# Kernel tuning notes

Measured on AMD Instinct MI355X. Metric: run time of the kernel, lower is better.

The kernel has to match this reference:

```python
import jax, jax.numpy as jnp
import numpy as np


def _conv(x, w, b, pad):
    y = jax.lax.conv_general_dilated(x, w, window_strides=(1, 1),
                                     padding=[(pad, pad), (pad, pad)],
                                     dimension_numbers=('NCHW', 'OIHW', 'NCHW'))
    return y + b[None, :, None, None]


def _kernel_normalizer(mask, k):
    # softmax over the k*k kernel taps; hamming=1 so the renorm is a numerical no-op (kept faithful)
    n, mck2, h, w = mask.shape
    mc = mck2 // (k * k)
    m = jax.nn.softmax(mask.reshape(n, mc, k * k, h, w), axis=2)
    m = m / jnp.sum(m, axis=2, keepdims=True)
    return m.reshape(n, mck2, h, w)


def _carafe(feat, mask, k, g, s):
    # CARAFE: out[n,c,i,j] = sum_{ki,kj} mask[n, grp*k*k + ki*k + kj, i, j] * feat[n, c, i//s+ki-r, j//s+kj-r]
    n, c, h, w = feat.shape
    r = (k - 1) // 2
    cg = c // g
    hs, ws = h * s, w * s
    pad = jnp.pad(feat, ((0, 0), (0, 0), (r, r), (r, r)))
    m = mask.reshape(n, g, k * k, hs, ws)
    out = jnp.zeros((n, g, cg, hs, ws), feat.dtype)
    idx = 0
    for ki in range(k):
        for kj in range(k):
            sh = pad[:, :, ki:ki + h, kj:kj + w]
            if s > 1:
                sh = jnp.repeat(jnp.repeat(sh, s, axis=2), s, axis=3)
            out = out + sh.reshape(n, g, cg, hs, ws) * m[:, :, idx][:, :, None]
            idx += 1
    return out.reshape(n, c, hs, ws)


def setup_inputs() -> dict:
    key = jax.random.key(0)
    ks = jax.random.split(key, 8)
    N, CH, CL, H, W, CC = 4, 256, 256, 128, 128, 64
    KL, KH, EK = 5, 3, 3

    def w_init(k, shape):
        fan_in = shape[1] * shape[2] * shape[3]
        return jax.random.normal(k, shape, jnp.float32) * (1.0 / np.sqrt(fan_in))

    return {
        'hr_feat': jax.random.normal(ks[0], (N, CH, H, W), jnp.float32),
        'lr_feat': jax.random.normal(ks[1], (N, CL, H // 2, W // 2), jnp.float32),
        'hr_w': w_init(ks[2], (CC, CH, 1, 1)), 'hr_b': jnp.zeros((CC,), jnp.float32),
        'lr_w': w_init(ks[3], (CC, CL, 1, 1)), 'lr_b': jnp.zeros((CC,), jnp.float32),
        'enc_w': w_init(ks[4], (KL * KL, CC, EK, EK)), 'enc_b': jnp.zeros((KL * KL,), jnp.float32),
        'enc2_w': w_init(ks[5], (KH * KH, CC, EK, EK)), 'enc2_b': jnp.zeros((KH * KH,), jnp.float32),
    }


def reference(hr_feat, lr_feat, hr_w, hr_b, lr_w, lr_b, enc_w, enc_b, enc2_w, enc2_b):
    KL, KH, G = 5, 3, 1
    chf = _conv(hr_feat, hr_w, hr_b, 0)
    clf = _conv(lr_feat, lr_w, lr_b, 0)
    mask_hr_hr = _conv(chf, enc2_w, enc2_b, 1)
    mask_hr_init = _kernel_normalizer(mask_hr_hr, KH)
    chf = chf + chf - _carafe(chf, mask_hr_init, KH, G, 1)
    mask_lr_hr = _conv(chf, enc_w, enc_b, 1)
    mask_lr_init = _kernel_normalizer(mask_lr_hr, KL)
    mask_lr_lr_lr = _conv(clf, enc_w, enc_b, 1)
    # carafe scale-2 output is already hr-sized -> F.interpolate(nearest, hr size) is identity
    mask_lr_lr = _carafe(mask_lr_lr_lr, mask_lr_init, KL, G, 2)
    mask_lr = mask_lr_hr + mask_lr_lr
    mask_lr_init = _kernel_normalizer(mask_lr, KL)
    mask_hr_lr = _carafe(_conv(clf, enc2_w, enc2_b, 1), mask_lr_init, KL, G, 2)
    mask_hr = mask_hr_hr + mask_hr_lr
    mask_lr_out = _kernel_normalizer(mask_lr, KL)
    lr_out = _carafe(lr_feat, mask_lr_out, KL, G, 2)
    mask_hr_out = _kernel_normalizer(mask_hr, KH)
    hr_out = (hr_feat - _carafe(hr_feat, mask_hr_out, KH, G, 1)) + hr_feat
    return (mask_lr_out, hr_out, lr_out)
```

## Files before the change

### kernel.cpp

```cpp
#include <hip/hip_runtime.h>
#include <hip/hip_bf16.h>

typedef __hip_bfloat16 bf16;

constexpr int Nn  = 4;
constexpr int Ci  = 256;
constexpr int Cc  = 64;
constexpr int Hh  = 128;
constexpr int Ww  = 128;
constexpr int HWh = Hh * Ww;
constexpr int Hl  = 64;
constexpr int Wl  = 64;
constexpr int HWl = Hl * Wl;
constexpr int K2L = 25;
constexpr int K2H = 9;

constexpr size_t OFF_MASK = 0;
constexpr size_t OFF_HR   = (size_t)Nn * K2L * HWh;
constexpr size_t OFF_LR   = OFF_HR + (size_t)Nn * Ci * HWh;

constexpr size_t A_CHF    = 0;
constexpr size_t A_MLRHR  = 0;
constexpr size_t A_MLRLL  = 4300000;
constexpr size_t A_CLFE2  = 4800000;
constexpr size_t A_MHRRAW = 5000000;
constexpr size_t A_WHR    = 7800000;
constexpr size_t A_WLR    = 7820000;
constexpr size_t A_WENC   = 7840000;
constexpr size_t A_WENC2  = 7860000;
constexpr size_t A_BHR    = 7870000;
constexpr size_t A_BLR    = 7870100;
constexpr size_t A_BENC   = 7870200;
constexpr size_t A_BENC2  = 7870300;

constexpr size_t B_CLF    = 0;
constexpr size_t B_CHF2   = 1100000;
constexpr size_t B_MHRHR  = 5300000;
constexpr size_t B_MLR    = 0;

__device__ __forceinline__ float tofloat(float v) { return v; }
__device__ __forceinline__ float tofloat(bf16 v) { return __bfloat162float(v); }

template<typename T> __device__ __forceinline__ T fromfloat(float v);
template<> __device__ __forceinline__ float fromfloat<float>(float v) { return v; }
template<> __device__ __forceinline__ bf16  fromfloat<bf16>(float v)  { return __float2bfloat16(v); }

__device__ __forceinline__ float* scrp(void* d, int f32, size_t reg, size_t off) {
  float* b = f32 ? ((float*)d + reg) : (float*)((bf16*)d + reg);
  return b + off;
}

__global__ void detect_dtype(const void* feat, int* flag) {
  __shared__ int s;
  if (threadIdx.x == 0) s = 0;
  __syncthreads();
  unsigned short b = ((const unsigned short*)feat)[threadIdx.x];
  float v = __uint_as_float(((unsigned int)b) << 16);
  if (!(fabsf(v) < 1000.0f)) atomicOr(&s, 1);
  __syncthreads();
  if (threadIdx.x == 0) *flag = s;
}

template<typename T>
__device__ void prep_body(const T* hw, const T* hb, const T* lw, const T* lb,
                          const T* ew, const T* eb, const T* e2w, const T* e2b,
                          float* whr, float* wlr, float* wenc, float* wenc2,
                          float* bhr, float* blr, float* benc, float* benc2) {
  int tid = blockIdx.x * 256 + threadIdx.x, nt = gridDim.x * 256;
  for (int i = tid; i < Cc * Ci; i += nt) {
    int co = i / Ci, ci = i % Ci;
    whr[ci * Cc + co] = tofloat(hw[i]);
    wlr[ci * Cc + co] = tofloat(lw[i]);
  }
  for (int i = tid; i < K2L * Cc * 9; i += nt) {
    int ko = i / (Cc * 9), r = i % (Cc * 9), ci = r / 9, k = r % 9;
    wenc[(ci * K2L + ko) * 9 + k] = tofloat(ew[i]);
  }
  for (int i = tid; i < K2H * Cc * 9; i += nt) {
    int ko = i / (Cc * 9), r = i % (Cc * 9), ci = r / 9, k = r % 9;
    wenc2[(ci * K2H + ko) * 9 + k] = tofloat(e2w[i]);
  }
  if (tid < Cc)  { bhr[tid] = tofloat(hb[tid]); blr[tid] = tofloat(lb[tid]); }
  if (tid < K2L) benc[tid]  = tofloat(eb[tid]);
  if (tid < K2H) benc2[tid] = tofloat(e2b[tid]);
}

__global__ void prep_weights(const int* flag, void* dout,
                             const void* hw, const void* hb, const void* lw, const void* lb,
                             const void* ew, const void* eb, const void* e2w, const void* e2b) {
  int f32 = *flag;
  float* whr   = scrp(dout, f32, OFF_LR, A_WHR);
  float* wlr   = scrp(dout, f32, OFF_LR, A_WLR);
  float* wenc  = scrp(dout, f32, OFF_LR, A_WENC);
  float* wenc2 = scrp(dout, f32, OFF_LR, A_WENC2);
  float* bhr   = scrp(dout, f32, OFF_LR, A_BHR);
  float* blr   = scrp(dout, f32, OFF_LR, A_BLR);
  float* benc  = scrp(dout, f32, OFF_LR, A_BENC);
  float* benc2 = scrp(dout, f32, OFF_LR, A_BENC2);
  if (f32) prep_body<float>((const float*)hw, (const float*)hb, (const float*)lw, (const float*)lb,
                            (const float*)ew, (const float*)eb, (const float*)e2w, (const float*)e2b,
                            whr, wlr, wenc, wenc2, bhr, blr, benc, benc2);
  else     prep_body<bf16>((const bf16*)hw, (const bf16*)hb, (const bf16*)lw, (const bf16*)lb,
                           (const bf16*)ew, (const bf16*)eb, (const bf16*)e2w, (const bf16*)e2b,
                           whr, wlr, wenc, wenc2, bhr, blr, benc, benc2);
}

template<typename T, int CW>
__device__ __forceinline__ void conv1x1_core(const T* __restrict__ in, const float* __restrict__ wt,
                                             const float* __restrict__ bias, float* __restrict__ out,
                                             int P, int n, int pbase, int co0) {
  const T* inp = in + (size_t)n * Ci * P + pbase;
  float acc0[CW], acc1[CW];
  #pragma unroll
  for (int c = 0; c < CW; ++c) { float b = bias[co0 + c]; acc0[c] = b; acc1[c] = b; }

  #pragma unroll 8
  for (int ci = 0; ci < Ci; ++ci) {
    float v0, v1;
    if (sizeof(T) == 2) {
      unsigned u = *reinterpret_cast<const unsigned*>(inp + (size_t)ci * P);
      v0 = __uint_as_float(u << 16);
      v1 = __uint_as_float(u & 0xffff0000u);
    } else {
      float2 f = *reinterpret_cast<const float2*>(inp + (size_t)ci * P);
      v0 = f.x; v1 = f.y;
    }
    const float* wr = wt + ci * Cc + co0;
    #pragma unroll
    for (int c = 0; c < CW; ++c) {
      float wv = wr[c];
      acc0[c] = fmaf(v0, wv, acc0[c]);
      acc1[c] = fmaf(v1, wv, acc1[c]);
    }
  }
  float* op = out + (size_t)n * Cc * P + pbase;
  #pragma unroll
  for (int c = 0; c < CW; ++c)
    *reinterpret_cast<float2*>(op + (size_t)(co0 + c) * P) = make_float2(acc0[c], acc1[c]);
}

template<int CW>
__global__ __launch_bounds__(256) void conv1x1_k(const int* flag, void* dout, const void* in,
                                                 size_t w_off, size_t b_off,
                                                 size_t o_reg, size_t o_off, int P) {
  int f32 = __builtin_amdgcn_readfirstlane(*flag);
  const float* wt   = scrp(dout, f32, OFF_LR, w_off);
  const float* bias = scrp(dout, f32, OFF_LR, b_off);
  float* out        = scrp(dout, f32, o_reg, o_off);
  const int tid = threadIdx.x;
  const int n = blockIdx.z;
  const int pbase = (blockIdx.x * 64 + (tid & 63)) * 2;
  const int co0 = __builtin_amdgcn_readfirstlane(blockIdx.y * 4 * CW + (tid >> 6) * CW);
  if (f32) conv1x1_core<float, CW>((const float*)in, wt, bias, out, P, n, pbase, co0);
  else     conv1x1_core<bf16, CW>((const bf16*)in, wt, bias, out, P, n, pbase, co0);
}

constexpr int STG_TOT = 16 * 324;
constexpr int NSTG    = 21;

template<int KO, int KOG>
__device__ __forceinline__ void conv3x3_body(const float* __restrict__ in,
                                             const float* __restrict__ wt,
                                             const float* __restrict__ bias,
                                             float* __restrict__ out,
                                             int hh, int ww, int n, int ko0,
                                             int bx, int by, float* tile) {
  const int tid = threadIdx.x;
  const int tx = tid & 15, ty = tid >> 4;
  const bool inter = (bx >= 16) && (by >= 16) && (bx + 32 <= ww) && (by + 32 <= hh);

  float acc[KOG];
  #pragma unroll
  for (int ko = 0; ko < KOG; ++ko) acc[ko] = bias[ko0 + ko];

  float rg[NSTG];
  #pragma unroll
  for (int j = 0; j < NSTG; ++j) {
    int i = tid + j * 256;
    if (i < STG_TOT) {
      int ci = i / 324, r = i % 324, yy = r / 18, xx = r % 18;
      int gy = by + yy - 1, gx = bx + xx - 1;
      float v = 0.f;
      if (inter || (gy >= 0 && gy < hh && gx >= 0 && gx < ww))
        v = in[(((size_t)n * Cc + ci) * hh + gy) * ww + gx];
      rg[j] = v;
    }
  }

  for (int cc = 0; cc < Cc; cc += 16) {
    __syncthreads();
    #pragma unroll
    for (int j = 0; j < NSTG; ++j) {
      int i = tid + j * 256;
      if (i < STG_TOT) tile[i] = rg[j];
    }
    __syncthreads();
    if (cc + 16 < Cc) {
      #pragma unroll
      for (int j = 0; j < NSTG; ++j) {
        int i = tid + j * 256;
        if (i < STG_TOT) {
          int ci = i / 324, r = i % 324, yy = r / 18, xx = r % 18;
          int gy = by + yy - 1, gx = bx + xx - 1;
          float v = 0.f;
          if (inter || (gy >= 0 && gy < hh && gx >= 0 && gx < ww))
            v = in[(((size_t)n * Cc + cc + 16 + ci) * hh + gy) * ww + gx];
          rg[j] = v;
        }
      }
    }
    for (int ci = 0; ci < 16; ++ci) {
      float nb[9];
      #pragma unroll
      for (int dy = 0; dy < 3; ++dy)
        #pragma unroll
        for (int dx = 0; dx < 3; ++dx)
          nb[dy * 3 + dx] = tile[ci * 324 + (ty + dy) * 18 + tx + dx];
      const float* wr = wt + ((size_t)(cc + ci) * KO + ko0) * 9;
      #pragma unroll
      for (int ko = 0; ko < KOG; ++ko)
        #pragma unroll
        for (int k = 0; k < 9; ++k)
          acc[ko] = fmaf(wr[ko * 9 + k], nb[k], acc[ko]);
    }
  }
  const size_t ob = (((size_t)n * KO + ko0) * hh + by + ty) * ww + bx + tx;
  #pragma unroll
  for (int ko = 0; ko < KOG; ++ko) out[ob + (size_t)ko * hh * ww] = acc[ko];
}

template<int KO, int KOG>
__global__ __launch_bounds__(256) void conv3x3_k(const int* flag, void* dout,
                                                 size_t i_reg, size_t i_off,
                                                 size_t w_off, size_t b_off,
                                                 size_t o_reg, size_t o_off, int hh, int ww) {
  const int f32 = __builtin_amdgcn_readfirstlane(*flag);
  const float* in   = scrp(dout, f32, i_reg, i_off);
  const float* wt   = scrp(dout, f32, OFF_LR, w_off);
  const float* bias = scrp(dout, f32, OFF_LR, b_off);
  float* out        = scrp(dout, f32, o_reg, o_off);

  constexpr int NG = KO / KOG;
  __shared__ float tile[STG_TOT];
  const int n = blockIdx.z / NG;
  const int ko0 = (blockIdx.z % NG) * KOG;
  conv3x3_body<KO, KOG>(in, wt, bias, out, hh, ww, n, ko0, blockIdx.x * 16, blockIdx.y * 16, tile);
}

__global__ __launch_bounds__(256) void conv3x3_dual_k(const int* flag, void* dout) {
  const int f32 = __builtin_amdgcn_readfirstlane(*flag);
  const float* clf   = scrp(dout, f32, OFF_HR, B_CLF);
  const float* wenc  = scrp(dout, f32, OFF_LR, A_WENC);
  const float* benc  = scrp(dout, f32, OFF_LR, A_BENC);
  const float* wenc2 = scrp(dout, f32, OFF_LR, A_WENC2);
  const float* benc2 = scrp(dout, f32, OFF_LR, A_BENC2);
  float* o_ll = scrp(dout, f32, OFF_LR, A_MLRLL);
  float* o_e2 = scrp(dout, f32, OFF_LR, A_CLFE2);
  __shared__ float tile[STG_TOT];
  const int z = blockIdx.z;
  const int g = z & 7, n = z >> 3;
  const int bx = blockIdx.x * 16, by = blockIdx.y * 16;
  if (g < 5) conv3x3_body<K2L, 5>(clf, wenc, benc, o_ll, Hl, Wl, n, g * 5, bx, by, tile);
  else       conv3x3_body<K2H, 3>(clf, wenc2, benc2, o_e2, Hl, Wl, n, (g - 5) * 3, bx, by, tile);
}

template<typename FT, typename OT, int FINAL, int SM>
__device__ void carafe1_body(const FT* __restrict__ feat, const float* __restrict__ mask,
                             void* dout, size_t out_reg, float* outscr, int C, int CPB) {
  const int tid = threadIdx.x;
  const int tx = tid & 15, ty = tid >> 4;
  const int bx = blockIdx.x * 16, by = blockIdx.y * 16;
  const int numCG = C / CPB;
  const int n = blockIdx.z / numCG, cg = blockIdx.z % numCG;
  const int x = bx + tx, y = by + ty;
  const bool inter = (bx >= 16) && (by >= 16) && (bx + 32 <= Ww) && (by + 32 <= Hh);

  float mv[9];
  #pragma unroll
  for (int k = 0; k < 9; ++k)
    mv[k] = mask[(((size_t)n * 9 + k) * Hh + y) * Ww + x];
  if (SM) {
    float m = -1e30f;
    #pragma unroll
    for (int k = 0; k < 9; ++k) m = fmaxf(m, mv[k]);
    float s = 0.f;
    #pragma unroll
    for (int k = 0; k < 9; ++k) { mv[k] = __expf(mv[k] - m); s += mv[k]; }
    const float inv = 1.0f / s;
    #pragma unroll
    for (int k = 0; k < 9; ++k) mv[k] *= inv;
  }

  const int c0 = cg * CPB;
  if (inter) {
    for (int c = c0; c < c0 + CPB; ++c) {
      const FT* fp = feat + ((size_t)n * C + c) * HWh + (size_t)y * Ww + x;
      float center = tofloat(fp[0]);
      float s = 0.f;
      #pragma unroll
      for (int dy = -1; dy <= 1; ++dy)
        #pragma unroll
        for (int dx = -1; dx <= 1; ++dx)
          s = fmaf(tofloat(fp[dy * Ww + dx]), mv[(dy + 1) * 3 + (dx + 1)], s);
      float r = 2.f * center - s;
      const size_t li = ((size_t)n * C + c) * HWh + (size_t)y * Ww + x;
      if (FINAL) ((OT*)dout)[out_reg + li] = fromfloat<OT>(r);
      else       outscr[li] = r;
    }
  } else {
    for (int c = c0; c < c0 + CPB; ++c) {
      const FT* fp = feat + ((size_t)n * C + c) * HWh;
      float s = 0.f, center = 0.f;
      #pragma unroll
      for (int dy = -1; dy <= 1; ++dy)
        #pragma unroll
        for (int dx = -1; dx <= 1; ++dx) {
          int yy = y + dy, xx = x + dx;
          float fv = 0.f;
          if (yy >= 0 && yy < Hh && xx >= 0 && xx < Ww) fv = tofloat(fp[yy * Ww + xx]);
          if (dy == 0 && dx == 0) center = fv;
          s = fmaf(fv, mv[(dy + 1) * 3 + (dx + 1)], s);
        }
      float r = 2.f * center - s;
      const size_t li = ((size_t)n * C + c) * HWh + (size_t)y * Ww + x;
      if (FINAL) ((OT*)dout)[out_reg + li] = fromfloat<OT>(r);
      else       outscr[li] = r;
    }
  }
}

__global__ __launch_bounds__(256) void carafe1_scr_k(const int* flag, void* dout,
    size_t f_reg, size_t f_off, size_t m_reg, size_t m_off, size_t o_reg, size_t o_off,
    int C, int CPB) {
  int f32 = __builtin_amdgcn_readfirstlane(*flag);
  carafe1_body<float, float, 0, 1>(scrp(dout, f32, f_reg, f_off), scrp(dout, f32, m_reg, m_off),
                                   dout, 0, scrp(dout, f32, o_reg, o_off), C, CPB);
}

__global__ __launch_bounds__(256) void carafe1_io_k(const int* flag, void* dout, const void* feat,
    size_t m_reg, size_t m_off, size_t out_reg, int C, int CPB) {
  int f32 = __builtin_amdgcn_readfirstlane(*flag);
  const float* m = scrp(dout, f32, m_reg, m_off);
  if (f32) carafe1_body<float, float, 1, 1>((const float*)feat, m, dout, out_reg, nullptr, C, CPB);
  else     carafe1_body<bf16, bf16, 1, 1>((const bf16*)feat, m, dout, out_reg, nullptr, C, CPB);
}

template<typename FT, typename MT, typename OT, typename MOT, int ADD, int FINAL, int SM, int WMASK>
__device__ void carafe2_body(const FT* __restrict__ feat, const MT* __restrict__ mask,
                             const float* __restrict__ addend, void* dout, size_t out_reg,
                             float* outscr, int C, int CPB) {
  __shared__ float ft[8][144];
  const int tid = threadIdx.x;
  const int tx = tid & 15, ty = tid >> 4;
  const int bx = blockIdx.x * 16, by = blockIdx.y * 16;
  const int numCG = C / CPB;
  const int n = blockIdx.z / numCG, cg = blockIdx.z % numCG;
  const int x = bx + tx, y = by + ty;
  const bool inter = (bx >= 16) && (by >= 16) && (bx + 32 <= Ww) && (by + 32 <= Hh);

  float mv[25];
  #pragma unroll
  for (int k = 0; k < 25; ++k)
    mv[k] = tofloat(mask[(((size_t)n * 25 + k) * Hh + y) * Ww + x]);
  if (SM) {
    float m = -1e30f;
    #pragma unroll
    for (int k = 0; k < 25; ++k) m = fmaxf(m, mv[k]);
    float s = 0.f;
    #pragma unroll
    for (int k = 0; k < 25; ++k) { mv[k] = __expf(mv[k] - m); s += mv[k]; }
    const float inv = 1.0f / s;
    #pragma unroll
    for (int k = 0; k < 25; ++k) mv[k] *= inv;
  }
  if (WMASK && cg == 0) {
    const size_t g = (size_t)n * 25 * HWh + (size_t)y * Ww + x;
    MOT* mo = (MOT*)dout;
    #pragma unroll
    for (int k = 0; k < 25; ++k) mo[g + (size_t)k * HWh] = fromfloat<MOT>(mv[k]);
  }

  const int fy0 = (by >> 1) - 2, fx0 = (bx >> 1) - 2;
  const int fyb = (ty >> 1) + 2, fxb = (tx >> 1) + 2;
  const int c0 = cg * CPB;

  for (int cb = 0; cb < CPB; cb += 8) {
    const int lim = (CPB - cb < 8) ? (CPB - cb) : 8;
    __syncthreads();
    if (inter) {
      for (int i = tid; i < lim * 144; i += 256) {
        int cc = i / 144, r = i % 144, fy = r / 12, fx = r % 12;
        ft[cc][r] = tofloat(feat[((size_t)n * C + c0 + cb + cc) * HWl + (fy0 + fy) * Wl + fx0 + fx]);
      }
    } else {
      for (int i = tid; i < lim * 144; i += 256) {
        int cc = i / 144, r = i % 144, fy = r / 12, fx = r % 12;
        int gy = fy0 + fy, gx = fx0 + fx;
        float v = 0.f;
        if (gy >= 0 && gy < Hl && gx >= 0 && gx < Wl)
          v = tofloat(feat[((size_t)n * C + c0 + cb + cc) * HWl + gy * Wl + gx]);
        ft[cc][r] = v;
      }
    }
    __syncthreads();
    for (int cc = 0; cc < lim; ++cc) {
      float s = 0.f;
      #pragma unroll
      for (int ki = 0; ki < 5; ++ki)
        #pragma unroll
        for (int kj = 0; kj < 5; ++kj)
          s = fmaf(ft[cc][(fyb + ki - 2) * 12 + (fxb + kj - 2)], mv[ki * 5 + kj], s);
      const size_t li = (((size_t)n * C + c0 + cb + cc) * Hh + y) * Ww + x;
      float r = ADD ? (addend[li] + s) : s;
      if (FINAL) ((OT*)dout)[out_reg + li] = fromfloat<OT>(r);
      else       outscr[li] = r;
    }
  }
}

__global__ __launch_bounds__(256) void carafe2_scr_k(const int* flag, void* dout,
    size_t f_reg, size_t f_off, size_t m_reg, size_t m_off, size_t a_reg, size_t a_off,
    size_t o_reg, size_t o_off, int C, int CPB) {
  int f32 = __builtin_amdgcn_readfirstlane(*flag);
  carafe2_body<float, float, float, float, 1, 0, 1, 0>(
      scrp(dout, f32, f_reg, f_off), scrp(dout, f32, m_reg, m_off),
      scrp(dout, f32, a_reg, a_off), dout, 0, scrp(dout, f32, o_reg, o_off), C, CPB);
}

__global__ __launch_bounds__(256) void carafe2_m0_k(const int* flag, void* dout,
    size_t f_reg, size_t f_off, size_t m_reg, size_t m_off, size_t a_reg, size_t a_off,
    size_t o_reg, size_t o_off, int C, int CPB) {
  int f32 = __builtin_amdgcn_readfirstlane(*flag);
  const float* f = scrp(dout, f32, f_reg, f_off);
  const float* m = scrp(dout, f32, m_reg, m_off);
  const float* a = scrp(dout, f32, a_reg, a_off);
  float* o = scrp(dout, f32, o_reg, o_off);
  if (f32) carafe2_body<float, float, float, float, 1, 0, 1, 1>(f, m, a, dout, 0, o, C, CPB);
  else     carafe2_body<float, float, float, bf16, 1, 0, 1, 1>(f, m, a, dout, 0, o, C, CPB);
}

__global__ __launch_bounds__(256) void carafe2_io_k(const int* flag, void* dout, const void* feat,
    size_t out_reg, int C, int CPB) {
  int f32 = __builtin_amdgcn_readfirstlane(*flag);
  if (f32) carafe2_body<float, float, float, float, 0, 1, 0, 0>((const float*)feat, (const float*)dout,
      nullptr, dout, out_reg, nullptr, C, CPB);
  else     carafe2_body<bf16, bf16, bf16, bf16, 0, 1, 0, 0>((const bf16*)feat, (const bf16*)dout,
      nullptr, dout, out_reg, nullptr, C, CPB);
}

extern "C" void kernel_launch(void* const* d_in, const int* in_sizes, int n_in,
                              void* d_out, int out_size, void* d_ws, size_t ws_size,
                              hipStream_t stream) {
  const void* hr_feat = d_in[0];
  const void* lr_feat = d_in[1];
  int* flag = (int*)d_ws;

  detect_dtype<<<1, 256, 0, stream>>>(hr_feat, flag);
  prep_weights<<<64, 256, 0, stream>>>(flag, d_out, d_in[2], d_in[3], d_in[4], d_in[5],
                                       d_in[6], d_in[7], d_in[8], d_in[9]);
  conv1x1_k<8><<<dim3(HWh / 128, 2, Nn), 256, 0, stream>>>(flag, d_out, hr_feat, A_WHR, A_BHR, OFF_LR, A_CHF, HWh);
  conv1x1_k<4><<<dim3(HWl / 128, 4, Nn), 256, 0, stream>>>(flag, d_out, lr_feat, A_WLR, A_BLR, OFF_HR, B_CLF, HWl);
  conv3x3_k<K2H, 3><<<dim3(8, 8, Nn * 3), 256, 0, stream>>>(flag, d_out, OFF_LR, A_CHF, A_WENC2, A_BENC2, OFF_HR, B_MHRHR, Hh, Ww);
  conv3x3_dual_k<<<dim3(4, 4, Nn * 8), 256, 0, stream>>>(flag, d_out);
  carafe1_scr_k<<<dim3(8, 8, Nn * (Cc / 16)), 256, 0, stream>>>(flag, d_out, OFF_LR, A_CHF, OFF_HR, B_MHRHR, OFF_HR, B_CHF2, Cc, 16);
  conv3x3_k<K2L, 5><<<dim3(8, 8, Nn * 5), 256, 0, stream>>>(flag, d_out, OFF_HR, B_CHF2, A_WENC, A_BENC, OFF_LR, A_MLRHR, Hh, Ww);
  carafe2_scr_k<<<dim3(8, 8, Nn * 5), 256, 0, stream>>>(flag, d_out, OFF_LR, A_MLRLL, OFF_LR, A_MLRHR,
                                                        OFF_LR, A_MLRHR, OFF_HR, B_MLR, K2L, 5);
  carafe2_m0_k<<<dim3(8, 8, Nn * 3), 256, 0, stream>>>(flag, d_out, OFF_LR, A_CLFE2,
                                                       OFF_HR, B_MLR, OFF_HR, B_MHRHR,
                                                       OFF_LR, A_MHRRAW, K2H, 3);
  carafe1_io_k<<<dim3(8, 8, Nn * (Ci / 32)), 256, 0, stream>>>(flag, d_out, hr_feat,
                                                               OFF_LR, A_MHRRAW, OFF_HR, Ci, 32);
  carafe2_io_k<<<dim3(8, 8, Nn * (Ci / 32)), 256, 0, stream>>>(flag, d_out, lr_feat, OFF_LR, Ci, 32);
}
```

Before: 537.1 us.

## Rewrite final CARAFE kernels to compute two pixels per thread with vector I/O

Replaces the two final-output CARAFE kernels with new versions in which each thread computes two horizontally adjacent output pixels. Feature, mask and output accesses use packed float2 or paired-bf16 loads and stores. The 3x3 kernel reads rows straight from global memory. The 5x5 scale-2 kernel stages a wider low-res tile in shared memory and shares each feature value between both pixels. The grids are reshaped to 32x16 tiles with 16 channels per block, which raises bytes per memory transaction and halves per-pixel mask and softmax overhead, at the cost of more registers per thread.

New measurement: 546.2 us. Within noise of the previous version (+1.7%).

```diff
diff --git a/kernel.cpp b/kernel.cpp
--- a/kernel.cpp
+++ b/kernel.cpp
@@ -44,6 +44,10 @@
 template<typename T> __device__ __forceinline__ T fromfloat(float v);
 template<> __device__ __forceinline__ float fromfloat<float>(float v) { return v; }
 template<> __device__ __forceinline__ bf16  fromfloat<bf16>(float v)  { return __float2bfloat16(v); }
+
+__device__ __forceinline__ unsigned short bfbits(bf16 v) {
+  return *reinterpret_cast<unsigned short*>(&v);
+}
 
 __device__ __forceinline__ float* scrp(void* d, int f32, size_t reg, size_t off) {
   float* b = f32 ? ((float*)d + reg) : (float*)((bf16*)d + reg);
@@ -337,12 +341,114 @@
                                    dout, 0, scrp(dout, f32, o_reg, o_off), C, CPB);
 }
 
-__global__ __launch_bounds__(256) void carafe1_io_k(const int* flag, void* dout, const void* feat,
+template<typename FT>
+__device__ void carafe1_io2_body(const FT* __restrict__ feat, const float* __restrict__ mask,
+                                 FT* __restrict__ outp, int C, int CPB) {
+  const int tid = threadIdx.x;
+  const int tx = tid & 15, ty = tid >> 4;
+  const int bx = blockIdx.x * 32, by = blockIdx.y * 16;
+  const int numCG = C / CPB;
+  const int n = blockIdx.z / numCG, cg = blockIdx.z % numCG;
+  const int x0 = bx + 2 * tx, y = by + ty;
+  const bool inter = (bx >= 2) && (by >= 1) && (bx + 34 <= Ww) && (by + 17 <= Hh);
+
+  float mv0[9], mv1[9];
+  #pragma unroll
+  for (int k = 0; k < 9; ++k) {
+    float2 m2 = *reinterpret_cast<const float2*>(mask + (((size_t)n * 9 + k) * Hh + y) * Ww + x0);
+    mv0[k] = m2.x; mv1[k] = m2.y;
+  }
+  {
+    float m = -1e30f;
+    #pragma unroll
+    for (int k = 0; k < 9; ++k) m = fmaxf(m, mv0[k]);
+    float s = 0.f;
+    #pragma unroll
+    for (int k = 0; k < 9; ++k) { mv0[k] = __expf(mv0[k] - m); s += mv0[k]; }
+    const float inv = 1.0f / s;
+    #pragma unroll
+    for (int k = 0; k < 9; ++k) mv0[k] *= inv;
+  }
+  {
+    float m = -1e30f;
+    #pragma unroll
+    for (int k = 0; k < 9; ++k) m = fmaxf(m, mv1[k]);
+    float s = 0.f;
+    #pragma unroll
+    for (int k = 0; k < 9; ++k) { mv1[k] = __expf(mv1[k] - m); s += mv1[k]; }
+    const float inv = 1.0f / s;
+    #pragma unroll
+    for (int k = 0; k < 9; ++k) mv1[k] *= inv;
+  }
+
+  const int c0 = cg * CPB;
+  if (inter) {
+    for (int c = c0; c < c0 + CPB; ++c) {
+      const FT* fp = feat + ((size_t)n * C + c) * HWh;
+      float s0 = 0.f, s1 = 0.f, c0v = 0.f, c1v = 0.f;
+      #pragma unroll
+      for (int dy = -1; dy <= 1; ++dy) {
+        const FT* rp = fp + (size_t)(y + dy) * Ww + x0 - 2;
+        float v[6];
+        if (sizeof(FT) == 2) {
+          const unsigned* up = reinterpret_cast<const unsigned*>(rp);
+          unsigned u0 = up[0], u1 = up[1], u2 = up[2];
+          v[0] = __uint_as_float(u0 << 16); v[1] = __uint_as_float(u0 & 0xffff0000u);
+          v[2] = __uint_as_float(u1 << 16); v[3] = __uint_as_float(u1 & 0xffff0000u);
+          v[4] = __uint_as_float(u2 << 16); v[5] = __uint_as_float(u2 & 0xffff0000u);
+        } else {
+          const float2* qp = reinterpret_cast<const float2*>(rp);
+          float2 a = qp[0], b = qp[1], cq = qp[2];
+          v[0] = a.x; v[1] = a.y; v[2] = b.x; v[3] = b.y; v[4] = cq.x; v[5] = cq.y;
+        }
+        if (dy == 0) { c0v = v[2]; c1v = v[3]; }
+        #pragma unroll
+        for (int dx = 0; dx < 3; ++dx) {
+          s0 = fmaf(v[1 + dx], mv0[(dy + 1) * 3 + dx], s0);
+          s1 = fmaf(v[2 + dx], mv1[(dy + 1) * 3 + dx], s1);
+        }
+      }
+      float r0 = 2.f * c0v - s0, r1 = 2.f * c1v - s1;
+      const size_t li = ((size_t)n * C + c) * HWh + (size_t)y * Ww + x0;
+      if (sizeof(FT) == 2) {
+        bf16 b0 = __float2bfloat16(r0), b1 = __float2bfloat16(r1);
+        *reinterpret_cast<unsigned*>(outp + li) =
+            (unsigned)bfbits(b0) | ((unsigned)bfbits(b1) << 16);
+      } else {
+        *reinterpret_cast<float2*>(outp + li) = make_float2(r0, r1);
+      }
+    }
+  } else {
+    for (int c = c0; c < c0 + CPB; ++c) {
+      const FT* fp = feat + ((size_t)n * C + c) * HWh;
+      #pragma unroll
+      for (int px = 0; px < 2; ++px) {
+        const int x = x0 + px;
+        float s = 0.f, center = 0.f;
+        #pragma unroll
+        for (int dy = -1; dy <= 1; ++dy)
+          #pragma unroll
+          for (int dx = -1; dx <= 1; ++dx) {
+            int yy = y + dy, xx = x + dx;
+            float fv = 0.f;
+            if (yy >= 0 && yy < Hh && xx >= 0 && xx < Ww) fv = tofloat(fp[yy * Ww + xx]);
+            if (dy == 0 && dx == 0) center = fv;
+            float mw = px ? mv1[(dy + 1) * 3 + (dx + 1)] : mv0[(dy + 1) * 3 + (dx + 1)];
+            s = fmaf(fv, mw, s);
+          }
+        float r = 2.f * center - s;
+        outp[((size_t)n * C + c) * HWh + (size_t)y * Ww + x] = fromfloat<FT>(r);
+      }
+    }
+  }
+}
+
+__global__ __launch_bounds__(256) void carafe1_io2_k(const int* flag, void* dout, const void* feat,
     size_t m_reg, size_t m_off, size_t out_reg, int C, int CPB) {
   int f32 = __builtin_amdgcn_readfirstlane(*flag);
   const float* m = scrp(dout, f32, m_reg, m_off);
-  if (f32) carafe1_body<float, float, 1, 1>((const float*)feat, m, dout, out_reg, nullptr, C, CPB);
-  else     carafe1_body<bf16, bf16, 1, 1>((const bf16*)feat, m, dout, out_reg, nullptr, C, CPB);
+  if (f32) carafe1_io2_body<float>((const float*)feat, m, (float*)dout + out_reg, C, CPB);
+  else     carafe1_io2_body<bf16>((const bf16*)feat, m, (bf16*)dout + out_reg, C, CPB);
 }
 
 template<typename FT, typename MT, typename OT, typename MOT, int ADD, int FINAL, int SM, int WMASK>
@@ -439,13 +545,93 @@
   else     carafe2_body<float, float, float, bf16, 1, 0, 1, 1>(f, m, a, dout, 0, o, C, CPB);
 }
 
-__global__ __launch_bounds__(256) void carafe2_io_k(const int* flag, void* dout, const void* feat,
+template<typename FT>
+__device__ void carafe2_io2_body(const FT* __restrict__ feat, const FT* __restrict__ maskO,
+                                 FT* __restrict__ outp, int C, int CPB) {
+  __shared__ float ft[8][240];
+  const int tid = threadIdx.x;
+  const int tx = tid & 15, ty = tid >> 4;
+  const int bx = blockIdx.x * 32, by = blockIdx.y * 16;
+  const int numCG = C / CPB;
+  const int n = blockIdx.z / numCG, cg = blockIdx.z % numCG;
+  const int x0 = bx + 2 * tx, y = by + ty;
+
+  float mv0[25], mv1[25];
+  #pragma unroll
+  for (int k = 0; k < 25; ++k) {
+    const FT* mp = maskO + (((size_t)n * 25 + k) * Hh + y) * Ww + x0;
+    if (sizeof(FT) == 2) {
+      unsigned u = *reinterpret_cast<const unsigned*>(mp);
+      mv0[k] = __uint_as_float(u << 16);
+      mv1[k] = __uint_as_float(u & 0xffff0000u);
+    } else {
+      float2 m2 = *reinterpret_cast<const float2*>(mp);
+      mv0[k] = m2.x; mv1[k] = m2.y;
+    }
+  }
+
+  const int fy0 = (by >> 1) - 2, fx0 = (bx >> 1) - 2;
+  const int fyb = (ty >> 1) + 2, fxc = tx + 2;
+  const int c0 = cg * CPB;
+  const bool stg_ok = (fy0 >= 0) && (fy0 + 12 <= Hl) && (fx0 >= 0) && (fx0 + 20 <= Wl);
+
+  for (int cb = 0; cb < CPB; cb += 8) {
+    const int lim = (CPB - cb < 8) ? (CPB - cb) : 8;
+    __syncthreads();
+    if (stg_ok) {
+      for (int i = tid; i < lim * 120; i += 256) {
+        int cc = i / 120, r = i % 120, fy = r / 10, fx2 = (r % 10) * 2;
+        const FT* sp = feat + ((size_t)n * C + c0 + cb + cc) * HWl + (size_t)(fy0 + fy) * Wl + fx0 + fx2;
+        float a, b;
+        if (sizeof(FT) == 2) {
+          unsigned u = *reinterpret_cast<const unsigned*>(sp);
+          a = __uint_as_float(u << 16);
+          b = __uint_as_float(u & 0xffff0000u);
+        } else {
+          float2 f2 = *reinterpret_cast<const float2*>(sp);
+          a = f2.x; b = f2.y;
+        }
+        ft[cc][fy * 20 + fx2]     = a;
+        ft[cc][fy * 20 + fx2 + 1] = b;
+      }
+    } else {
+      for (int i = tid; i < lim * 240; i += 256) {
+        int cc = i / 240, r = i % 240, fy = r / 20, fx = r % 20;
+        int gy = fy0 + fy, gx = fx0 + fx;
+        float v = 0.f;
+        if (gy >= 0 && gy < Hl && gx >= 0 && gx < Wl)
+          v = tofloat(feat[((size_t)n * C + c0 + cb + cc) * HWl + (size_t)gy * Wl + gx]);
+        ft[cc][r] = v;
+      }
+    }
+    __syncthreads();
+    for (int cc = 0; cc < lim; ++cc) {
+      float s0 = 0.f, s1 = 0.f;
+      #pragma unroll
+      for (int ki = 0; ki < 5; ++ki)
+        #pragma unroll
+        for (int kj = 0; kj < 5; ++kj) {
+          float fv = ft[cc][(fyb + ki - 2) * 20 + (fxc + kj - 2)];
+          s0 = fmaf(fv, mv0[ki * 5 + kj], s0);
+          s1 = fmaf(fv, mv1[ki * 5 + kj], s1);
+        }
+      const size_t li = (((size_t)n * C + c0 + cb + cc) * Hh + y) * Ww + x0;
+      if (sizeof(FT) == 2) {
+        bf16 b0 = __float2bfloat16(s0), b1 = __float2bfloat16(s1);
+        *reinterpret_cast<unsigned*>(outp + li) =
+            (unsigned)bfbits(b0) | ((unsigned)bfbits(b1) << 16);
+      } else {
+        *reinterpret_cast<float2*>(outp + li) = make_float2(s0, s1);
+      }
+    }
+  }
+}
+
+__global__ __launch_bounds__(256) void carafe2_io2_k(const int* flag, void* dout, const void* feat,
     size_t out_reg, int C, int CPB) {
   int f32 = __builtin_amdgcn_readfirstlane(*flag);
-  if (f32) carafe2_body<float, float, float, float, 0, 1, 0, 0>((const float*)feat, (const float*)dout,
-      nullptr, dout, out_reg, nullptr, C, CPB);
-  else     carafe2_body<bf16, bf16, bf16, bf16, 0, 1, 0, 0>((const bf16*)feat, (const bf16*)dout,
-      nullptr, dout, out_reg, nullptr, C, CPB);
+  if (f32) carafe2_io2_body<float>((const float*)feat, (const float*)dout, (float*)dout + out_reg, C, CPB);
+  else     carafe2_io2_body<bf16>((const bf16*)feat, (const bf16*)dout, (bf16*)dout + out_reg, C, CPB);
 }
 
 extern "C" void kernel_launch(void* const* d_in, const int* in_sizes, int n_in,
@@ -469,7 +655,7 @@
   carafe2_m0_k<<<dim3(8, 8, Nn * 3), 256, 0, stream>>>(flag, d_out, OFF_LR, A_CLFE2,
                                                        OFF_HR, B_MLR, OFF_HR, B_MHRHR,
                                                        OFF_LR, A_MHRRAW, K2H, 3);
-  carafe1_io_k<<<dim3(8, 8, Nn * (Ci / 32)), 256, 0, stream>>>(flag, d_out, hr_feat,
-                                                               OFF_LR, A_MHRRAW, OFF_HR, Ci, 32);
-  carafe2_io_k<<<dim3(8, 8, Nn * (Ci / 32)), 256, 0, stream>>>(flag, d_out, lr_feat, OFF_LR, Ci, 32);
-}
+  carafe1_io2_k<<<dim3(Ww / 32, Hh / 16, Nn * (Ci / 16)), 256, 0, stream>>>(flag, d_out, hr_feat,
+                                                                            OFF_LR, A_MHRRAW, OFF_HR, Ci, 16);
+  carafe2_io2_k<<<dim3(Ww / 32, Hh / 16, Nn * (Ci / 16)), 256, 0, stream>>>(flag, d_out, lr_feat, OFF_LR, Ci, 16);
+}
```
